# Performance work log

Hardware: AMD Instinct MI355X
Metric: run time of the kernel (lower is better)

The kernel has to match this reference:

```python
import jax, jax.numpy as jnp
import numpy as np

K, P, Q, D = 16, 1024, 1024, 64  # heads, value-in dim, out dim, head dim; P'=P, Q'=Q, D'=D
B, N = 2, 2048                   # batch, seq (self-attention: M=N)
TEMPERATURE = jnp.sqrt(jnp.float32(D))

def _xavier(key, shape):
    fan_in, fan_out = shape[-2], shape[-1]
    lim = jnp.sqrt(6.0 / (fan_in + fan_out))
    return jax.random.uniform(key, shape, jnp.float32, -lim, lim)

def setup_inputs() -> dict:
    key = jax.random.key(0)
    k0, k1, k2, k3, k4 = jax.random.split(key, 5)
    return {
        'y_prime': jax.random.normal(k0, (B, N, Q), jnp.float32),
        'mask': jnp.zeros((N, N), jnp.float32),  # log-domain additive mask [M,N]
        'Lam_x': _xavier(k1, (K, P, D)),  # Lambda^(x): [K,P',D']
        'Lam_y': _xavier(k2, (K, Q, D)),  # Lambda^(y): [K,Q',D']
        'Th_x': _xavier(k3, (K, P, D)),   # Theta^(x):  [K,P,D]
        'Th_y': _xavier(k4, (K, Q, D)),   # Theta^(y):  [K,Q,D]
    }

def reference(y_prime, mask, Lam_x, Lam_y, Th_x, Th_y):
    # self-attention: x' = x = y'
    x_p = y_prime
    x = x_p
    # key projection: [B,M,K,D']
    r = jnp.einsum('bmp,kpd->bmkd', x_p, Lam_x)
    # bilinear scores: [K,B,M,N]
    r = jnp.einsum('bmkd,kqd,bnq->kbmn', r, Lam_y, y_prime)
    r = r + mask[None, None, :, :]
    # softmax over M (axis=-2), scaled by sqrt(D')
    A = jax.nn.softmax(r / TEMPERATURE, axis=-2)
    # value aggregation: [B,N,K,D]
    r = jnp.einsum('kbmn,bmp,kpd->bnkd', A, x, Th_x)
    # output projection: [B,N,Q]
    return jnp.einsum('bnkd,kqd->bnq', r, Th_y)
```

## Files before the change

kernel.cpp:

```cpp
#include <hip/hip_runtime.h>
#include <hip/hip_bf16.h>

#define KH 16
#define PD 1024
#define QD 1024
#define DD 64
#define BB 2
#define NN 2048
#define BN 4096
#define ST 72
#define SOFT_C 12.0f

typedef unsigned short u16;
typedef __attribute__((ext_vector_type(8))) short bf16x8;
typedef __attribute__((ext_vector_type(4))) short bf16x4;
typedef __attribute__((ext_vector_type(4))) float f32x4;

__device__ __forceinline__ float bf2f(u16 u) {
    return __uint_as_float(((unsigned)u) << 16);
}
__device__ __forceinline__ u16 f2bf(float f) {
    unsigned x = __float_as_uint(f);
    x += 0x7FFFu + ((x >> 16) & 1u);
    return (u16)(x >> 16);
}
__device__ __forceinline__ f32x4 mfma_k32(bf16x8 a, bf16x8 b, f32x4 c) {
    return __builtin_amdgcn_mfma_f32_16x16x32_bf16(a, b, c, 0, 0, 0);
}
__device__ __forceinline__ f32x4 mfma_k16(bf16x4 a, bf16x4 b, f32x4 c) {
#if __has_builtin(__builtin_amdgcn_mfma_f32_16x16x16bf16_1k)
    return __builtin_amdgcn_mfma_f32_16x16x16bf16_1k(a, b, c, 0, 0, 0);
#else
    asm("v_mfma_f32_16x16x16_bf16 %0, %1, %2, %0" : "+v"(c) : "v"(a), "v"(b));
    return c;
#endif
}
__device__ __forceinline__ bf16x8 ldfrag(const u16* base, int r0, int kc, int lane) {
    return *reinterpret_cast<const bf16x8*>(base + (r0 + (lane & 15)) * ST + kc +
                                            ((lane >> 4) << 3));
}
__device__ __forceinline__ bf16x4 ldfrag4(const u16* base, int r0, int kc, int lane) {
    return *reinterpret_cast<const bf16x4*>(base + (r0 + (lane & 15)) * ST + kc +
                                            ((lane >> 4) << 2));
}
__device__ __forceinline__ bf16x8 ldfragL(const u16* base, int r0, int kc, int lane) {
    return *reinterpret_cast<const bf16x8*>(base + ((r0 + (lane & 15)) << 6) + kc +
                                            ((lane >> 4) << 3));
}
__device__ __forceinline__ bf16x4 pack4(float a, float b, float c, float d) {
    union { bf16x4 v; __hip_bfloat162 h[2]; } u;
    u.h[0] = __float22bfloat162_rn(make_float2(a, b));
    u.h[1] = __float22bfloat162_rn(make_float2(c, d));
    return u.v;
}
__device__ __forceinline__ void gl_lds16(const u16* g, u16* l) {
    __builtin_amdgcn_global_load_lds(
        (const __attribute__((address_space(1))) void*)g,
        (__attribute__((address_space(3))) void*)l, 16, 0, 0);
}
template <int ROWS>
__device__ __forceinline__ void stage_dma(const u16* __restrict__ src, int ld,
                                          u16* dst, int lane, int w) {
#pragma unroll
    for (int c = 0; c < ROWS / 32; ++c) {
        int rbase = (w * (ROWS / 32) + c) * 8;
        const u16* g = src + (size_t)(rbase + (lane >> 3)) * ld + ((lane & 7) << 3);
        gl_lds16(g, dst + (rbase << 6));
    }
}
template <int ROWS, int NT>
__device__ __forceinline__ void stage_rows(const u16* __restrict__ src, int ld,
                                           u16* dst, int tid) {
#pragma unroll
    for (int it = 0; it < ROWS * 8 / NT; ++it) {
        int chunk = it * NT + tid;
        int row = chunk >> 3, col = (chunk & 7) << 3;
        *reinterpret_cast<uint4*>(dst + row * ST + col) =
            *reinterpret_cast<const uint4*>(src + row * ld + col);
    }
}

__global__ void detect_kernel(const u16* __restrict__ y, int* flag, int* mnz) {
    __shared__ int cnt;
    if (threadIdx.x == 0) cnt = 0;
    __syncthreads();
    int local = 0;
    for (int i = threadIdx.x; i < 8192; i += 256) {
        u16 u = y[i];
        int e = (u >> 7) & 0xFF;
        if (u == 0 || (e >= 96 && e < 160)) local++;
    }
    atomicAdd(&cnt, local);
    __syncthreads();
    if (threadIdx.x == 0) {
        *flag = (cnt > 7372) ? 1 : 0;
        *mnz = 0;
    }
}

__global__ __launch_bounds__(256) void mcheck_kernel(const void* __restrict__ msrc,
                                                     const int* __restrict__ flag,
                                                     int* mnz) {
    size_t n4 = (size_t)NN * NN / 8;
    if (*flag == 0) n4 *= 2;
    const uint4* p = (const uint4*)msrc;
    unsigned acc = 0;
    for (size_t i = blockIdx.x * 256 + threadIdx.x; i < n4;
         i += (size_t)gridDim.x * 256) {
        uint4 v = p[i];
        acc |= v.x | v.y | v.z | v.w;
    }
    if (acc) atomicOr(mnz, 1);
}

__global__ __launch_bounds__(256) void convert_kernel(
    const void* __restrict__ src, u16* __restrict__ dst, int n,
    const int* __restrict__ flag) {
    int i = (blockIdx.x * 256 + threadIdx.x) * 4;
    if (i >= n) return;
    if (*flag) {
        *reinterpret_cast<uint2*>(dst + i) =
            *reinterpret_cast<const uint2*>((const u16*)src + i);
    } else {
        float4 f = *reinterpret_cast<const float4*>((const float*)src + i);
        u16 t[4] = {f2bf(f.x), f2bf(f.y), f2bf(f.z), f2bf(f.w)};
        *reinterpret_cast<uint2*>(dst + i) = *reinterpret_cast<uint2*>(t);
    }
}

__global__ __launch_bounds__(256) void maskc_kernel(const void* __restrict__ src,
                                                    u16* __restrict__ dst,
                                                    const int* __restrict__ flag,
                                                    const int* __restrict__ mnz) {
    if (*mnz == 0) return;
    size_t i = ((size_t)blockIdx.x * 256 + threadIdx.x) * 8;
    float f[8];
    if (*flag) {
        uint4 v = *reinterpret_cast<const uint4*>((const u16*)src + i);
        u16 t[8];
        *reinterpret_cast<uint4*>(t) = v;
#pragma unroll
        for (int e = 0; e < 8; ++e) f[e] = bf2f(t[e]);
    } else {
        float4 a = *reinterpret_cast<const float4*>((const float*)src + i);
        float4 b = *reinterpret_cast<const float4*>((const float*)src + i + 4);
        f[0] = a.x; f[1] = a.y; f[2] = a.z; f[3] = a.w;
        f[4] = b.x; f[5] = b.y; f[6] = b.z; f[7] = b.w;
    }
    u16 t[8];
#pragma unroll
    for (int e = 0; e < 8; ++e) t[e] = f2bf(f[e] * 0.125f);
    *reinterpret_cast<uint4*>(dst + i) = *reinterpret_cast<uint4*>(t);
}

__global__ __launch_bounds__(256) void convtr_kernel(const void* __restrict__ src,
                                                     u16* __restrict__ dst,
                                                     float scale,
                                                     const int* __restrict__ flag) {
    int k = blockIdx.y, p0 = blockIdx.x * 64;
    int tid = threadIdx.x;
    __shared__ float T[64][65];
    int isbf = *flag;
    const u16* s16 = (const u16*)src + ((size_t)k * PD + p0) * DD;
    const float* s32 = (const float*)src + ((size_t)k * PD + p0) * DD;
#pragma unroll
    for (int it = 0; it < 2; ++it) {
        int chunk = it * 256 + tid;
        int row = chunk >> 3, c8 = (chunk & 7) << 3;
        float f[8];
        if (isbf) {
            uint4 v = *reinterpret_cast<const uint4*>(s16 + row * DD + c8);
            u16 t[8];
            *reinterpret_cast<uint4*>(t) = v;
#pragma unroll
            for (int e = 0; e < 8; ++e) f[e] = bf2f(t[e]);
        } else {
            float4 a = *reinterpret_cast<const float4*>(s32 + row * DD + c8);
            float4 b = *reinterpret_cast<const float4*>(s32 + row * DD + c8 + 4);
            f[0] = a.x; f[1] = a.y; f[2] = a.z; f[3] = a.w;
            f[4] = b.x; f[5] = b.y; f[6] = b.z; f[7] = b.w;
        }
#pragma unroll
        for (int e = 0; e < 8; ++e) T[row][c8 + e] = f[e] * scale;
    }
    __syncthreads();
    u16* drow = dst + (size_t)k * DD * PD + p0;
#pragma unroll
    for (int it = 0; it < 2; ++it) {
        int chunk = it * 256 + tid;
        int d = chunk >> 3, c8 = (chunk & 7) << 3;
        u16 t[8];
#pragma unroll
        for (int e = 0; e < 8; ++e) t[e] = f2bf(T[c8 + e][d]);
        *reinterpret_cast<uint4*>(drow + (size_t)d * PD + c8) =
            *reinterpret_cast<uint4*>(t);
    }
}

__global__ __launch_bounds__(256) void thyr_kernel(const void* __restrict__ src,
                                                   u16* __restrict__ dst,
                                                   const int* __restrict__ flag) {
    int k = blockIdx.y, q0 = blockIdx.x * 64;
    int tid = threadIdx.x, isbf = *flag;
#pragma unroll
    for (int it = 0; it < 2; ++it) {
        int chunk = it * 256 + tid;
        int row = chunk >> 3, c8 = (chunk & 7) << 3;
        size_t si = ((size_t)k * QD + q0 + row) * DD + c8;
        u16 t[8];
        if (isbf) {
            *reinterpret_cast<uint4*>(t) =
                *reinterpret_cast<const uint4*>((const u16*)src + si);
        } else {
            float4 a = *reinterpret_cast<const float4*>((const float*)src + si);
            float4 b = *reinterpret_cast<const float4*>((const float*)src + si + 4);
            t[0] = f2bf(a.x); t[1] = f2bf(a.y); t[2] = f2bf(a.z); t[3] = f2bf(a.w);
            t[4] = f2bf(b.x); t[5] = f2bf(b.y); t[6] = f2bf(b.z); t[7] = f2bf(b.w);
        }
        *reinterpret_cast<uint4*>(dst + (size_t)(q0 + row) * (KH * DD) + k * DD + c8) =
            *reinterpret_cast<uint4*>(t);
    }
}

__global__ __launch_bounds__(256, 3) void proj_gemm(
    const u16* __restrict__ A,
    const u16* __restrict__ Bm,
    u16* __restrict__ Xk, u16* __restrict__ Yk, u16* __restrict__ Vtg) {
    int tid = threadIdx.x, lane = tid & 63, w = tid >> 6;
    int mhalf = w & 1, nhalf = w >> 1;
    int m0 = blockIdx.x * 128, n0 = blockIdx.y * 128;
    __shared__ u16 As[128 * 64];
    __shared__ u16 Bs[128 * 64];
    f32x4 acc[4][4] = {};

    for (int kk = 0; kk < PD; kk += 64) {
        __syncthreads();
        stage_dma<128>(A + (size_t)m0 * PD + kk, PD, As, lane, w);
        stage_dma<128>(Bm + (size_t)n0 * PD + kk, PD, Bs, lane, w);
        __syncthreads();
#pragma unroll
        for (int kc = 0; kc < 64; kc += 32) {
            bf16x8 af[4], bf[4];
#pragma unroll
            for (int i = 0; i < 4; ++i) af[i] = ldfragL(As, mhalf * 64 + i * 16, kc, lane);
#pragma unroll
            for (int j = 0; j < 4; ++j) bf[j] = ldfragL(Bs, nhalf * 64 + j * 16, kc, lane);
#pragma unroll
            for (int i = 0; i < 4; ++i)
#pragma unroll
                for (int j = 0; j < 4; ++j) acc[i][j] = mfma_k32(af[i], bf[j], acc[i][j]);
        }
    }
    int nsel = n0 + nhalf * 64;
    int s = nsel >> 10, kh = (nsel >> 6) & 15;
    int quad = lane >> 4, col = lane & 15;
    if (s == 2) {
        u16* vb = Vtg + (size_t)kh * DD * BN;
#pragma unroll
        for (int i = 0; i < 4; ++i)
#pragma unroll
            for (int j = 0; j < 4; ++j) {
                int d = j * 16 + col;
                int mrow = m0 + mhalf * 64 + i * 16 + quad * 4;
                *reinterpret_cast<bf16x4*>(vb + (size_t)d * BN + mrow) =
                    pack4(acc[i][j][0], acc[i][j][1], acc[i][j][2], acc[i][j][3]);
            }
    } else {
        u16* ob = (s == 0 ? Xk : Yk) + (size_t)kh * BN * DD;
#pragma unroll
        for (int i = 0; i < 4; ++i)
#pragma unroll
            for (int j = 0; j < 4; ++j)
#pragma unroll
                for (int reg = 0; reg < 4; ++reg) {
                    int mrow = m0 + mhalf * 64 + i * 16 + quad * 4 + reg;
                    ob[(size_t)mrow * DD + j * 16 + col] = f2bf(acc[i][j][reg]);
                }
    }
}

__global__ __launch_bounds__(128, 3) void attn_kernel(
    const u16* __restrict__ Xk,
    const u16* __restrict__ Yk,
    const u16* __restrict__ Vtg,
    const u16* __restrict__ maskc,
    const int* __restrict__ mnz,
    u16* __restrict__ O) {
    int tid = threadIdx.x, lane = tid & 63, w = tid >> 6;
    int quad = lane >> 4, col = lane & 15;
    int q0 = blockIdx.x * 64, k = blockIdx.y, b = blockIdx.z;
    const u16* Qp = Yk + ((size_t)k * BN + b * NN + q0) * DD;
    const u16* Kp = Xk + ((size_t)k * BN + b * NN) * DD;
    const u16* Vp = Vtg + (size_t)k * DD * BN + b * NN;
    __shared__ u16 Qs[64 * ST];
    __shared__ u16 Ks[64 * ST];
    __shared__ u16 Vt[64 * ST];
    int mz = *mnz;

    stage_rows<64, 128>(Qp, DD, Qs, tid);
    __syncthreads();
    bf16x8 qf[2][2];
#pragma unroll
    for (int g = 0; g < 2; ++g)
#pragma unroll
        for (int kc = 0; kc < 2; ++kc)
            qf[g][kc] = ldfrag(Qs, w * 32 + g * 16, kc * 32, lane);

    float lp[2] = {0.0f, 0.0f};
    f32x4 oacc[2][4] = {};

    for (int m0 = 0; m0 < NN; m0 += 64) {
        __syncthreads();
        stage_rows<64, 128>(Kp + (size_t)m0 * DD, DD, Ks, tid);
        stage_rows<64, 128>(Vp + m0, BN, Vt, tid);
        __syncthreads();

        f32x4 sacc[2][4] = {};
#pragma unroll
        for (int kg = 0; kg < 4; ++kg) {
            bf16x8 a0 = ldfrag(Ks, kg * 16, 0, lane);
            bf16x8 a1 = ldfrag(Ks, kg * 16, 32, lane);
#pragma unroll
            for (int g = 0; g < 2; ++g) {
                sacc[g][kg] = mfma_k32(a0, qf[g][0], sacc[g][kg]);
                sacc[g][kg] = mfma_k32(a1, qf[g][1], sacc[g][kg]);
            }
        }
        if (mz) {
#pragma unroll
            for (int g = 0; g < 2; ++g)
#pragma unroll
                for (int kg = 0; kg < 4; ++kg)
#pragma unroll
                    for (int reg = 0; reg < 4; ++reg)
                        sacc[g][kg][reg] += bf2f(
                            maskc[(size_t)(m0 + kg * 16 + quad * 4 + reg) * NN +
                                  q0 + w * 32 + g * 16 + col]);
        }
        bf16x4 pb[2][4];
#pragma unroll
        for (int g = 0; g < 2; ++g)
#pragma unroll
            for (int kg = 0; kg < 4; ++kg) {
                float p0 = __expf(sacc[g][kg][0] - SOFT_C);
                float p1 = __expf(sacc[g][kg][1] - SOFT_C);
                float p2 = __expf(sacc[g][kg][2] - SOFT_C);
                float p3 = __expf(sacc[g][kg][3] - SOFT_C);
                lp[g] += (p0 + p1) + (p2 + p3);
                pb[g][kg] = pack4(p0, p1, p2, p3);
            }
#pragma unroll
        for (int kg = 0; kg < 4; ++kg)
#pragma unroll
            for (int dg = 0; dg < 4; ++dg) {
                bf16x4 av = ldfrag4(Vt, dg * 16, kg * 16, lane);
#pragma unroll
                for (int g = 0; g < 2; ++g)
                    oacc[g][dg] = mfma_k16(av, pb[g][kg], oacc[g][dg]);
            }
    }

    float inv[2];
#pragma unroll
    for (int g = 0; g < 2; ++g) {
        float l = lp[g];
        l += __shfl_xor(l, 16);
        l += __shfl_xor(l, 32);
        inv[g] = 1.0f / l;
    }
#pragma unroll
    for (int g = 0; g < 2; ++g)
#pragma unroll
        for (int dg = 0; dg < 4; ++dg)
            *reinterpret_cast<bf16x4*>(Qs + (w * 32 + g * 16 + col) * ST + dg * 16 +
                                       quad * 4) =
                pack4(oacc[g][dg][0] * inv[g], oacc[g][dg][1] * inv[g],
                      oacc[g][dg][2] * inv[g], oacc[g][dg][3] * inv[g]);
    __syncthreads();
#pragma unroll
    for (int it = 0; it < 4; ++it) {
        int chunk = it * 128 + tid;
        int row = chunk >> 3, c8 = (chunk & 7) << 3;
        *reinterpret_cast<uint4*>(O + (size_t)(b * NN + q0 + row) * (KH * DD) +
                                  k * DD + c8) =
            *reinterpret_cast<const uint4*>(Qs + row * ST + c8);
    }
}

__global__ __launch_bounds__(256, 3) void out_gemm(
    const u16* __restrict__ A,
    const u16* __restrict__ Bm,
    const int* __restrict__ flag,
    void* __restrict__ outv) {
    int tid = threadIdx.x, lane = tid & 63, w = tid >> 6;
    int mhalf = w & 1, nhalf = w >> 1;
    int m0 = blockIdx.x * 128, n0 = blockIdx.y * 128;
    __shared__ u16 As[128 * 64];
    __shared__ u16 Bs[128 * 64];
    f32x4 acc[4][4] = {};

    for (int kk = 0; kk < KH * DD; kk += 64) {
        __syncthreads();
        stage_dma<128>(A + (size_t)m0 * (KH * DD) + kk, KH * DD, As, lane, w);
        stage_dma<128>(Bm + (size_t)n0 * (KH * DD) + kk, KH * DD, Bs, lane, w);
        __syncthreads();
#pragma unroll
        for (int kc = 0; kc < 64; kc += 32) {
            bf16x8 af[4], bf[4];
#pragma unroll
            for (int i = 0; i < 4; ++i) af[i] = ldfragL(As, mhalf * 64 + i * 16, kc, lane);
#pragma unroll
            for (int j = 0; j < 4; ++j) bf[j] = ldfragL(Bs, nhalf * 64 + j * 16, kc, lane);
#pragma unroll
            for (int i = 0; i < 4; ++i)
#pragma unroll
                for (int j = 0; j < 4; ++j) acc[i][j] = mfma_k32(af[i], bf[j], acc[i][j]);
        }
    }
    int isbf = *flag;
    int quad = lane >> 4, col = lane & 15;
#pragma unroll
    for (int i = 0; i < 4; ++i)
#pragma unroll
        for (int j = 0; j < 4; ++j)
#pragma unroll
            for (int reg = 0; reg < 4; ++reg) {
                size_t row = m0 + mhalf * 64 + i * 16 + quad * 4 + reg;
                int c = n0 + nhalf * 64 + j * 16 + col;
                if (isbf)
                    ((u16*)outv)[row * QD + c] = f2bf(acc[i][j][reg]);
                else
                    ((float*)outv)[row * QD + c] = acc[i][j][reg];
            }
}

extern "C" void kernel_launch(void* const* d_in, const int* in_sizes, int n_in,
                              void* d_out, int out_size, void* d_ws, size_t ws_size,
                              hipStream_t stream) {
    char* wsb = (char*)d_ws;
    int* flag = (int*)wsb;
    int* mnz = (int*)(wsb + 16);
    u16* ycan = (u16*)(wsb + 64);
    const size_t NYP = (size_t)BN * PD;
    const size_t NW = (size_t)KH * PD * DD;
    u16* Wcat = ycan + NYP;
    u16* LamXt = Wcat;
    u16* LamYt = Wcat + NW;
    u16* ThXt = Wcat + 2 * NW;
    u16* ThYr = Wcat + 3 * NW;
    u16* Xk = ThYr + NW;
    u16* Yk = Xk + (size_t)KH * BN * DD;
    u16* Vtg = Yk + (size_t)KH * BN * DD;
    u16* maskc = Vtg + (size_t)KH * BN * DD;
    u16* Ob = ycan;

    detect_kernel<<<1, 256, 0, stream>>>((const u16*)d_in[0], flag, mnz);
    mcheck_kernel<<<256, 256, 0, stream>>>(d_in[1], flag, mnz);
    convert_kernel<<<(int)(NYP / 1024), 256, 0, stream>>>(d_in[0], ycan, (int)NYP, flag);
    convtr_kernel<<<dim3(PD / 64, KH), 256, 0, stream>>>(d_in[2], LamXt, 1.0f, flag);
    convtr_kernel<<<dim3(PD / 64, KH), 256, 0, stream>>>(d_in[3], LamYt, 0.125f, flag);
    convtr_kernel<<<dim3(PD / 64, KH), 256, 0, stream>>>(d_in[4], ThXt, 1.0f, flag);
    thyr_kernel<<<dim3(QD / 64, KH), 256, 0, stream>>>(d_in[5], ThYr, flag);
    maskc_kernel<<<2048, 256, 0, stream>>>(d_in[1], maskc, flag, mnz);

    proj_gemm<<<dim3(BN / 128, 3072 / 128), 256, 0, stream>>>(ycan, Wcat, Xk, Yk, Vtg);
    attn_kernel<<<dim3(NN / 64, KH, BB), 128, 0, stream>>>(Xk, Yk, Vtg, maskc, mnz, Ob);
    out_gemm<<<dim3(BN / 128, QD / 128), 256, 0, stream>>>(Ob, ThYr, flag, d_out);
}
```

Baseline: 248.3 us.

## Split attention over key range, widen blocks, and merge weight-prep launches

The attention kernel now uses 256-thread blocks covering 128 query rows and can split the softmax-sum dimension (M) into two halves across extra grid blocks. Each half writes a normalized partial output and its row sums, and a new combine kernel merges them with sum-weighted averaging. The three transpose-convert launches and the Theta_y reorder are fused into one launch. The split aims to raise parallelism and K/V reuse per block, at the cost of extra workspace, an extra pass over the output, and one more bf16 rounding of the partial outputs. The split only runs if the workspace is large enough.

Result: no change. 244.9 us (-1.4%).

```diff
diff --git a/kernel.cpp b/kernel.cpp
--- a/kernel.cpp
+++ b/kernel.cpp
@@ -153,72 +153,73 @@
     *reinterpret_cast<uint4*>(dst + i) = *reinterpret_cast<uint4*>(t);
 }
 
-__global__ __launch_bounds__(256) void convtr_kernel(const void* __restrict__ src,
-                                                     u16* __restrict__ dst,
-                                                     float scale,
-                                                     const int* __restrict__ flag) {
-    int k = blockIdx.y, p0 = blockIdx.x * 64;
-    int tid = threadIdx.x;
-    __shared__ float T[64][65];
+__global__ __launch_bounds__(256) void prew_kernel(
+    const void* __restrict__ s0, const void* __restrict__ s1,
+    const void* __restrict__ s2, const void* __restrict__ s3,
+    u16* __restrict__ LamXt, u16* __restrict__ LamYt, u16* __restrict__ ThXt,
+    u16* __restrict__ ThYr, const int* __restrict__ flag) {
+    int z = blockIdx.z, k = blockIdx.y, tid = threadIdx.x;
     int isbf = *flag;
-    const u16* s16 = (const u16*)src + ((size_t)k * PD + p0) * DD;
-    const float* s32 = (const float*)src + ((size_t)k * PD + p0) * DD;
-#pragma unroll
-    for (int it = 0; it < 2; ++it) {
-        int chunk = it * 256 + tid;
-        int row = chunk >> 3, c8 = (chunk & 7) << 3;
-        float f[8];
-        if (isbf) {
-            uint4 v = *reinterpret_cast<const uint4*>(s16 + row * DD + c8);
+    if (z < 3) {
+        const void* src = (z == 0) ? s0 : (z == 1) ? s1 : s2;
+        u16* dst = (z == 0) ? LamXt : (z == 1) ? LamYt : ThXt;
+        float scale = (z == 1) ? 0.125f : 1.0f;
+        int p0 = blockIdx.x * 64;
+        __shared__ float T[64][65];
+        const u16* s16 = (const u16*)src + ((size_t)k * PD + p0) * DD;
+        const float* s32 = (const float*)src + ((size_t)k * PD + p0) * DD;
+#pragma unroll
+        for (int it = 0; it < 2; ++it) {
+            int chunk = it * 256 + tid;
+            int row = chunk >> 3, c8 = (chunk & 7) << 3;
+            float f[8];
+            if (isbf) {
+                uint4 v = *reinterpret_cast<const uint4*>(s16 + row * DD + c8);
+                u16 t[8];
+                *reinterpret_cast<uint4*>(t) = v;
+#pragma unroll
+                for (int e = 0; e < 8; ++e) f[e] = bf2f(t[e]);
+            } else {
+                float4 a = *reinterpret_cast<const float4*>(s32 + row * DD + c8);
+                float4 b = *reinterpret_cast<const float4*>(s32 + row * DD + c8 + 4);
+                f[0] = a.x; f[1] = a.y; f[2] = a.z; f[3] = a.w;
+                f[4] = b.x; f[5] = b.y; f[6] = b.z; f[7] = b.w;
+            }
+#pragma unroll
+            for (int e = 0; e < 8; ++e) T[row][c8 + e] = f[e] * scale;
+        }
+        __syncthreads();
+        u16* drow = dst + (size_t)k * DD * PD + p0;
+#pragma unroll
+        for (int it = 0; it < 2; ++it) {
+            int chunk = it * 256 + tid;
+            int d = chunk >> 3, c8 = (chunk & 7) << 3;
             u16 t[8];
-            *reinterpret_cast<uint4*>(t) = v;
-#pragma unroll
-            for (int e = 0; e < 8; ++e) f[e] = bf2f(t[e]);
-        } else {
-            float4 a = *reinterpret_cast<const float4*>(s32 + row * DD + c8);
-            float4 b = *reinterpret_cast<const float4*>(s32 + row * DD + c8 + 4);
-            f[0] = a.x; f[1] = a.y; f[2] = a.z; f[3] = a.w;
-            f[4] = b.x; f[5] = b.y; f[6] = b.z; f[7] = b.w;
-        }
-#pragma unroll
-        for (int e = 0; e < 8; ++e) T[row][c8 + e] = f[e] * scale;
-    }
-    __syncthreads();
-    u16* drow = dst + (size_t)k * DD * PD + p0;
-#pragma unroll
-    for (int it = 0; it < 2; ++it) {
-        int chunk = it * 256 + tid;
-        int d = chunk >> 3, c8 = (chunk & 7) << 3;
-        u16 t[8];
-#pragma unroll
-        for (int e = 0; e < 8; ++e) t[e] = f2bf(T[c8 + e][d]);
-        *reinterpret_cast<uint4*>(drow + (size_t)d * PD + c8) =
-            *reinterpret_cast<uint4*>(t);
-    }
-}
-
-__global__ __launch_bounds__(256) void thyr_kernel(const void* __restrict__ src,
-                                                   u16* __restrict__ dst,
-                                                   const int* __restrict__ flag) {
-    int k = blockIdx.y, q0 = blockIdx.x * 64;
-    int tid = threadIdx.x, isbf = *flag;
-#pragma unroll
-    for (int it = 0; it < 2; ++it) {
-        int chunk = it * 256 + tid;
-        int row = chunk >> 3, c8 = (chunk & 7) << 3;
-        size_t si = ((size_t)k * QD + q0 + row) * DD + c8;
-        u16 t[8];
-        if (isbf) {
-            *reinterpret_cast<uint4*>(t) =
-                *reinterpret_cast<const uint4*>((const u16*)src + si);
-        } else {
-            float4 a = *reinterpret_cast<const float4*>((const float*)src + si);
-            float4 b = *reinterpret_cast<const float4*>((const float*)src + si + 4);
-            t[0] = f2bf(a.x); t[1] = f2bf(a.y); t[2] = f2bf(a.z); t[3] = f2bf(a.w);
-            t[4] = f2bf(b.x); t[5] = f2bf(b.y); t[6] = f2bf(b.z); t[7] = f2bf(b.w);
-        }
-        *reinterpret_cast<uint4*>(dst + (size_t)(q0 + row) * (KH * DD) + k * DD + c8) =
-            *reinterpret_cast<uint4*>(t);
+#pragma unroll
+            for (int e = 0; e < 8; ++e) t[e] = f2bf(T[c8 + e][d]);
+            *reinterpret_cast<uint4*>(drow + (size_t)d * PD + c8) =
+                *reinterpret_cast<uint4*>(t);
+        }
+    } else {
+        int q0 = blockIdx.x * 64;
+#pragma unroll
+        for (int it = 0; it < 2; ++it) {
+            int chunk = it * 256 + tid;
+            int row = chunk >> 3, c8 = (chunk & 7) << 3;
+            size_t si = ((size_t)k * QD + q0 + row) * DD + c8;
+            u16 t[8];
+            if (isbf) {
+                *reinterpret_cast<uint4*>(t) =
+                    *reinterpret_cast<const uint4*>((const u16*)s3 + si);
+            } else {
+                float4 a = *reinterpret_cast<const float4*>((const float*)s3 + si);
+                float4 b = *reinterpret_cast<const float4*>((const float*)s3 + si + 4);
+                t[0] = f2bf(a.x); t[1] = f2bf(a.y); t[2] = f2bf(a.z); t[3] = f2bf(a.w);
+                t[4] = f2bf(b.x); t[5] = f2bf(b.y); t[6] = f2bf(b.z); t[7] = f2bf(b.w);
+            }
+            *reinterpret_cast<uint4*>(ThYr + (size_t)(q0 + row) * (KH * DD) +
+                                      k * DD + c8) = *reinterpret_cast<uint4*>(t);
+        }
     }
 }
 
@@ -279,25 +280,29 @@
     }
 }
 
-__global__ __launch_bounds__(128, 3) void attn_kernel(
+__global__ __launch_bounds__(256, 4) void attn_kernel(
     const u16* __restrict__ Xk,
     const u16* __restrict__ Yk,
     const u16* __restrict__ Vtg,
     const u16* __restrict__ maskc,
     const int* __restrict__ mnz,
-    u16* __restrict__ O) {
+    int mlen,
+    u16* __restrict__ Op0,
+    u16* __restrict__ Op1,
+    float* __restrict__ lbuf) {
     int tid = threadIdx.x, lane = tid & 63, w = tid >> 6;
     int quad = lane >> 4, col = lane & 15;
-    int q0 = blockIdx.x * 64, k = blockIdx.y, b = blockIdx.z;
+    int q0 = blockIdx.x * 128, k = blockIdx.y;
+    int z = blockIdx.z, b = z & 1, s = z >> 1;
     const u16* Qp = Yk + ((size_t)k * BN + b * NN + q0) * DD;
     const u16* Kp = Xk + ((size_t)k * BN + b * NN) * DD;
     const u16* Vp = Vtg + (size_t)k * DD * BN + b * NN;
-    __shared__ u16 Qs[64 * ST];
+    __shared__ u16 Qs[128 * ST];
     __shared__ u16 Ks[64 * ST];
     __shared__ u16 Vt[64 * ST];
     int mz = *mnz;
 
-    stage_rows<64, 128>(Qp, DD, Qs, tid);
+    stage_rows<128, 256>(Qp, DD, Qs, tid);
     __syncthreads();
     bf16x8 qf[2][2];
 #pragma unroll
@@ -309,10 +314,11 @@
     float lp[2] = {0.0f, 0.0f};
     f32x4 oacc[2][4] = {};
 
-    for (int m0 = 0; m0 < NN; m0 += 64) {
-        __syncthreads();
-        stage_rows<64, 128>(Kp + (size_t)m0 * DD, DD, Ks, tid);
-        stage_rows<64, 128>(Vp + m0, BN, Vt, tid);
+    int mbeg = s * mlen;
+    for (int m0 = mbeg; m0 < mbeg + mlen; m0 += 64) {
+        __syncthreads();
+        stage_rows<64, 256>(Kp + (size_t)m0 * DD, DD, Ks, tid);
+        stage_rows<64, 256>(Vp + m0, BN, Vt, tid);
         __syncthreads();
 
         f32x4 sacc[2][4] = {};
@@ -360,13 +366,21 @@
             }
     }
 
-    float inv[2];
+    float inv[2], lfull[2];
 #pragma unroll
     for (int g = 0; g < 2; ++g) {
         float l = lp[g];
         l += __shfl_xor(l, 16);
         l += __shfl_xor(l, 32);
+        lfull[g] = l;
         inv[g] = 1.0f / l;
+    }
+    u16* Od = s ? Op1 : Op0;
+    if (quad == 0) {
+#pragma unroll
+        for (int g = 0; g < 2; ++g)
+            lbuf[(size_t)s * (BN * KH) +
+                 (size_t)(b * NN + q0 + w * 32 + g * 16 + col) * KH + k] = lfull[g];
     }
 #pragma unroll
     for (int g = 0; g < 2; ++g)
@@ -377,14 +391,32 @@
                 pack4(oacc[g][dg][0] * inv[g], oacc[g][dg][1] * inv[g],
                       oacc[g][dg][2] * inv[g], oacc[g][dg][3] * inv[g]);
     __syncthreads();
-#pragma unroll
-    for (int it = 0; it < 4; ++it) {
-        int chunk = it * 128 + tid;
-        int row = chunk >> 3, c8 = (chunk & 7) << 3;
-        *reinterpret_cast<uint4*>(O + (size_t)(b * NN + q0 + row) * (KH * DD) +
-                                  k * DD + c8) =
-            *reinterpret_cast<const uint4*>(Qs + row * ST + c8);
-    }
+    int r = tid >> 1, h = tid & 1;
+    const u16* srow = Qs + r * ST + h * 32;
+    u16* drow = Od + (size_t)(b * NN + q0 + r) * (KH * DD) + k * DD + h * 32;
+#pragma unroll
+    for (int u = 0; u < 4; ++u)
+        *reinterpret_cast<uint4*>(drow + u * 8) =
+            *reinterpret_cast<const uint4*>(srow + u * 8);
+}
+
+__global__ __launch_bounds__(256) void comb_kernel(u16* __restrict__ Op0,
+                                                   const u16* __restrict__ Op1,
+                                                   const float* __restrict__ lbuf) {
+    size_t idx = ((size_t)blockIdx.x * 256 + threadIdx.x) * 8;
+    size_t row = idx >> 10;
+    int k = (int)((idx >> 6) & 15);
+    float l0 = lbuf[row * KH + k];
+    float l1 = lbuf[(size_t)BN * KH + row * KH + k];
+    float w0 = l0 / (l0 + l1), w1 = 1.0f - w0;
+    uint4 v0 = *reinterpret_cast<const uint4*>(Op0 + idx);
+    uint4 v1 = *reinterpret_cast<const uint4*>(Op1 + idx);
+    u16 a[8], b[8], o[8];
+    *reinterpret_cast<uint4*>(a) = v0;
+    *reinterpret_cast<uint4*>(b) = v1;
+#pragma unroll
+    for (int e = 0; e < 8; ++e) o[e] = f2bf(w0 * bf2f(a[e]) + w1 * bf2f(b[e]));
+    *reinterpret_cast<uint4*>(Op0 + idx) = *reinterpret_cast<uint4*>(o);
 }
 
 __global__ __launch_bounds__(256, 3) void out_gemm(
@@ -443,27 +475,31 @@
     u16* ycan = (u16*)(wsb + 64);
     const size_t NYP = (size_t)BN * PD;
     const size_t NW = (size_t)KH * PD * DD;
+    const size_t OSZ = (size_t)BN * KH * DD;
     u16* Wcat = ycan + NYP;
-    u16* LamXt = Wcat;
-    u16* LamYt = Wcat + NW;
-    u16* ThXt = Wcat + 2 * NW;
     u16* ThYr = Wcat + 3 * NW;
     u16* Xk = ThYr + NW;
-    u16* Yk = Xk + (size_t)KH * BN * DD;
-    u16* Vtg = Yk + (size_t)KH * BN * DD;
-    u16* maskc = Vtg + (size_t)KH * BN * DD;
+    u16* Yk = Xk + OSZ;
+    u16* Vtg = Yk + OSZ;
+    u16* maskc = Vtg + OSZ;
+    u16* Op1 = maskc + (size_t)NN * NN;
+    float* lbuf = (float*)(Op1 + OSZ);
     u16* Ob = ycan;
+
+    size_t need2 = (size_t)((char*)(lbuf + 2 * (size_t)BN * KH) - wsb);
+    int nsplit = (ws_size >= need2) ? 2 : 1;
 
     detect_kernel<<<1, 256, 0, stream>>>((const u16*)d_in[0], flag, mnz);
     mcheck_kernel<<<256, 256, 0, stream>>>(d_in[1], flag, mnz);
     convert_kernel<<<(int)(NYP / 1024), 256, 0, stream>>>(d_in[0], ycan, (int)NYP, flag);
-    convtr_kernel<<<dim3(PD / 64, KH), 256, 0, stream>>>(d_in[2], LamXt, 1.0f, flag);
-    convtr_kernel<<<dim3(PD / 64, KH), 256, 0, stream>>>(d_in[3], LamYt, 0.125f, flag);
-    convtr_kernel<<<dim3(PD / 64, KH), 256, 0, stream>>>(d_in[4], ThXt, 1.0f, flag);
-    thyr_kernel<<<dim3(QD / 64, KH), 256, 0, stream>>>(d_in[5], ThYr, flag);
+    prew_kernel<<<dim3(16, KH, 4), 256, 0, stream>>>(
+        d_in[2], d_in[3], d_in[4], d_in[5], Wcat, Wcat + NW, Wcat + 2 * NW, ThYr, flag);
     maskc_kernel<<<2048, 256, 0, stream>>>(d_in[1], maskc, flag, mnz);
 
     proj_gemm<<<dim3(BN / 128, 3072 / 128), 256, 0, stream>>>(ycan, Wcat, Xk, Yk, Vtg);
-    attn_kernel<<<dim3(NN / 64, KH, BB), 128, 0, stream>>>(Xk, Yk, Vtg, maskc, mnz, Ob);
+    attn_kernel<<<dim3(NN / 128, KH, BB * nsplit), 256, 0, stream>>>(
+        Xk, Yk, Vtg, maskc, mnz, NN / nsplit, Ob, Op1, lbuf);
+    if (nsplit == 2)
+        comb_kernel<<<(int)(OSZ / 8 / 256), 256, 0, stream>>>(Ob, Op1, lbuf);
     out_gemm<<<dim3(BN / 128, QD / 128), 256, 0, stream>>>(Ob, ThYr, flag, d_out);
 }
```
